# Performance work log

Hardware: AMD Instinct MI355X
Metric: run time of the kernel (lower is better)

## Reference

```python
import jax, jax.numpy as jnp
import numpy as np

E, M, K, I, TOPK = 8, 4096, 2048, 1408, 2
N = 2 * I  # gated: w1 produces [gate, up]


def setup_inputs() -> dict:
    key = jax.random.key(0)
    k1, k2, k3, k4, k5 = jax.random.split(key, 5)
    hidden_states = jax.random.normal(k1, (M, K), dtype=jnp.float32)
    w1 = jax.random.normal(k2, (E, N, K), dtype=jnp.float32) * 0.02
    w2 = jax.random.normal(k3, (E, K, I), dtype=jnp.float32) * 0.02
    raw = jax.random.uniform(k4, (M, TOPK), dtype=jnp.float32)
    topk_weights = raw / jnp.sum(raw, axis=-1, keepdims=True)  # router probs
    topk_ids = jax.random.randint(k5, (M, TOPK), 0, E, dtype=jnp.int32)
    return {
        "hidden_states": hidden_states,
        "w1": w1,
        "w2": w2,
        "topk_weights": topk_weights,
        "topk_ids": topk_ids,
    }


def reference(hidden_states, w1, w2, topk_weights, topk_ids):
    # MoE: permute -> grouped GEMM1 -> silu_and_mul -> grouped GEMM2 -> unpermute+reduce.
    # Dense-per-expert formulation (math-equivalent to grouped GEMM over routed tokens).
    # GEMM1: [E, M, N]
    h1 = jnp.einsum("mk,enk->emn", hidden_states, w1)
    gate, up = h1[..., :I], h1[..., I:]
    act = jax.nn.silu(gate) * up  # silu_and_mul, [E, M, I]
    # GEMM2: [E, M, K]
    y = jnp.einsum("emi,eki->emk", act, w2)
    # Unpermute: gather each token's topk expert outputs, apply router weights, reduce.
    y_tok = jnp.transpose(y, (1, 0, 2))  # [M, E, K]
    sel = jnp.take_along_axis(y_tok, topk_ids[:, :, None].astype(jnp.int32), axis=1)  # [M, topk, K]
    out = jnp.sum(sel * topk_weights[:, :, None], axis=1)  # [M, K]
    return out
```

## Files before the change

kernel.cpp:

```cpp
#include <hip/hip_runtime.h>
#include <hip/hip_bf16.h>
#include <stdint.h>

#define EXPERTS 8
#define MTOK 4096
#define KDIM 2048
#define IDIM 1408
#define NDIM 2816
#define CAP  8192

typedef __attribute__((ext_vector_type(8))) short bf16x8;
typedef __attribute__((ext_vector_type(4))) float f32x4;

__device__ __forceinline__ unsigned short f2bf(float x) {
    unsigned u = __float_as_uint(x);
    u = u + 0x7fffu + ((u >> 16) & 1u);
    return (unsigned short)(u >> 16);
}

__device__ __forceinline__ void gload16(const void* g, void* l) {
    __builtin_amdgcn_global_load_lds(
        (const __attribute__((address_space(1))) void*)g,
        (__attribute__((address_space(3))) void*)l, 16, 0, 0);
}

__global__ void __launch_bounds__(256) conv_bf16(const float* __restrict__ src,
                                                 unsigned short* __restrict__ dst, int n4) {
    int i = blockIdx.x * 256 + threadIdx.x;
    int st = gridDim.x * 256;
    for (; i < n4; i += st) {
        float4 v = reinterpret_cast<const float4*>(src)[i];
        ushort4 r;
        r.x = f2bf(v.x); r.y = f2bf(v.y); r.z = f2bf(v.z); r.w = f2bf(v.w);
        reinterpret_cast<ushort4*>(dst)[i] = r;
    }
}

__global__ void __launch_bounds__(256) router(const float* __restrict__ tw,
                                              const int* __restrict__ ids,
                                              int* __restrict__ tok, float* __restrict__ wgt,
                                              int* __restrict__ cnt) {
    int m = blockIdx.x * 256 + threadIdx.x;
    if (m >= MTOK) return;
#pragma unroll
    for (int t = 0; t < 2; t++) {
        int e = ids[m * 2 + t];
        int slot = atomicAdd(&cnt[e], 1);
        tok[e * CAP + slot] = m;
        wgt[e * CAP + slot] = tw[m * 2 + t];
    }
}

__global__ void scan_off(const int* __restrict__ cnt, int* __restrict__ off) {
    if (threadIdx.x == 0) {
        int s = 0;
        for (int e = 0; e < EXPERTS; e++) { off[e] = s; s += cnt[e]; }
    }
}


__global__ void __launch_bounds__(256) gemm1_silu(
    const unsigned short* __restrict__ hsb,
    const unsigned short* __restrict__ w1b,
    const int* __restrict__ tok,
    const int* __restrict__ cnt,
    const int* __restrict__ off,
    unsigned short* __restrict__ act) {
    const int bid = blockIdx.x;
    const int e = bid & 7;
    const int j = bid >> 3;
    const int rb = j / 22;
    const int cb = j - rb * 22;
    const int cnt_e = cnt[e];
    if (rb * 128 >= cnt_e) return;
    const int off_e = off[e];

    __shared__ unsigned short As[128 * 64];
    __shared__ unsigned short Bs[128 * 64];
    __shared__ int toks[128];

    const int tid = threadIdx.x;
    const int w = tid >> 6, lane = tid & 63;
    if (tid < 128) {
        int slot = rb * 128 + tid;
        toks[tid] = (slot < cnt_e) ? tok[e * CAP + slot] : 0;
    }
    __syncthreads();

    size_t sA[4], sB[4]; int dD[4];
    const size_t w1base = (size_t)e * NDIM * KDIM;
#pragma unroll
    for (int c = 0; c < 4; c++) {
        int i = c * 256 + tid;
        int row = i >> 3, g = (i & 7) ^ (row & 7);
        sA[c] = (size_t)toks[row] * KDIM + g * 8;
        int G = row >> 4;
        int wrow = ((G & 1) ? IDIM : 0) + cb * 64 + (G >> 1) * 16 + (row & 15);
        sB[c] = w1base + (size_t)wrow * KDIM + g * 8;
        dD[c] = i * 16;
    }

    const int wr = w >> 1, wc = w & 1;
    const int l16 = lane & 15, lg = lane >> 4;

    f32x4 acc[4][4];
#pragma unroll
    for (int m = 0; m < 4; m++)
#pragma unroll
        for (int n = 0; n < 4; n++) acc[m][n] = {0.f, 0.f, 0.f, 0.f};

    char* Ab = (char*)As;
    char* Bb = (char*)Bs;

    for (int kt = 0; kt < KDIM / 64; ++kt) {
        const int kof = kt * 64;
#pragma unroll
        for (int c = 0; c < 4; c++) gload16(hsb + sA[c] + kof, Ab + dD[c]);
#pragma unroll
        for (int c = 0; c < 4; c++) gload16(w1b + sB[c] + kof, Bb + dD[c]);
        __syncthreads();

#pragma unroll
        for (int h = 0; h < 2; h++) {
            bf16x8 a[4], b[4];
#pragma unroll
            for (int m = 0; m < 4; m++) {
                int r = wr * 64 + m * 16 + l16;
                a[m] = *reinterpret_cast<bf16x8*>(Ab + r * 128 + (((h * 4 + lg) ^ (r & 7)) * 16));
            }
#pragma unroll
            for (int n = 0; n < 4; n++) {
                int r = wc * 64 + n * 16 + l16;
                b[n] = *reinterpret_cast<bf16x8*>(Bb + r * 128 + (((h * 4 + lg) ^ (r & 7)) * 16));
            }
#pragma unroll
            for (int m = 0; m < 4; m++)
#pragma unroll
                for (int n = 0; n < 4; n++)
                    acc[m][n] = __builtin_amdgcn_mfma_f32_16x16x32_bf16(a[m], b[n], acc[m][n], 0, 0, 0);
        }
        __syncthreads();
    }

#pragma unroll
    for (int m = 0; m < 4; m++) {
#pragma unroll
        for (int np = 0; np < 2; np++) {
            f32x4 g4 = acc[m][np * 2];
            f32x4 u4 = acc[m][np * 2 + 1];
            int icol = cb * 64 + (wc * 2 + np) * 16 + l16;
#pragma unroll
            for (int j2 = 0; j2 < 4; j2++) {
                int grow = rb * 128 + wr * 64 + m * 16 + lg * 4 + j2;
                if (grow < cnt_e) {
                    float gt = g4[j2], up = u4[j2];
                    float s = gt / (1.f + __expf(-gt));
                    act[(size_t)(off_e + grow) * IDIM + icol] = f2bf(s * up);
                }
            }
        }
    }
}

__global__ void __launch_bounds__(256) gemm2_scatter(
    const unsigned short* __restrict__ act,
    const unsigned short* __restrict__ w2b,
    const int* __restrict__ tok,
    const float* __restrict__ wgt,
    const int* __restrict__ cnt,
    const int* __restrict__ off,
    float* __restrict__ out) {
    const int bid = blockIdx.x;
    const int e = bid & 7;
    const int j = bid >> 3;
    const int rb = j >> 4;
    const int cb = j & 15;
    const int cnt_e = cnt[e];
    if (rb * 128 >= cnt_e) return;
    const int off_e = off[e];

    __shared__ unsigned short As[128 * 64];
    __shared__ unsigned short Bs[128 * 64];
    __shared__ int toks[128];
    __shared__ float wgts[128];

    const int tid = threadIdx.x;
    const int w = tid >> 6, lane = tid & 63;
    if (tid < 128) {
        int slot = rb * 128 + tid;
        bool v = slot < cnt_e;
        toks[tid] = v ? tok[e * CAP + slot] : 0;
        wgts[tid] = v ? wgt[e * CAP + slot] : 0.f;
    }
    __syncthreads();

    size_t sA[4], sB[4]; int dD[4];
    const size_t w2base = (size_t)e * KDIM * IDIM;
#pragma unroll
    for (int c = 0; c < 4; c++) {
        int i = c * 256 + tid;
        int row = i >> 3, g = (i & 7) ^ (row & 7);
        int s = rb * 128 + row;
        sA[c] = (size_t)(off_e + (s < cnt_e ? s : 0)) * IDIM + g * 8;
        sB[c] = w2base + (size_t)(cb * 128 + row) * IDIM + g * 8;
        dD[c] = i * 16;
    }

    const int wr = w >> 1, wc = w & 1;
    const int l16 = lane & 15, lg = lane >> 4;

    f32x4 acc[4][4];
#pragma unroll
    for (int m = 0; m < 4; m++)
#pragma unroll
        for (int n = 0; n < 4; n++) acc[m][n] = {0.f, 0.f, 0.f, 0.f};

    char* Ab = (char*)As;
    char* Bb = (char*)Bs;

    for (int kt = 0; kt < IDIM / 64; ++kt) {
        const int kof = kt * 64;
#pragma unroll
        for (int c = 0; c < 4; c++) gload16(act + sA[c] + kof, Ab + dD[c]);
#pragma unroll
        for (int c = 0; c < 4; c++) gload16(w2b + sB[c] + kof, Bb + dD[c]);
        __syncthreads();

#pragma unroll
        for (int h = 0; h < 2; h++) {
            bf16x8 a[4], b[4];
#pragma unroll
            for (int m = 0; m < 4; m++) {
                int r = wr * 64 + m * 16 + l16;
                a[m] = *reinterpret_cast<bf16x8*>(Ab + r * 128 + (((h * 4 + lg) ^ (r & 7)) * 16));
            }
#pragma unroll
            for (int n = 0; n < 4; n++) {
                int r = wc * 64 + n * 16 + l16;
                b[n] = *reinterpret_cast<bf16x8*>(Bb + r * 128 + (((h * 4 + lg) ^ (r & 7)) * 16));
            }
#pragma unroll
            for (int m = 0; m < 4; m++)
#pragma unroll
                for (int n = 0; n < 4; n++)
                    acc[m][n] = __builtin_amdgcn_mfma_f32_16x16x32_bf16(a[m], b[n], acc[m][n], 0, 0, 0);
        }
        __syncthreads();
    }

#pragma unroll
    for (int m = 0; m < 4; m++) {
#pragma unroll
        for (int n = 0; n < 4; n++) {
            int kcol = cb * 128 + wc * 64 + n * 16 + l16;
#pragma unroll
            for (int j2 = 0; j2 < 4; j2++) {
                int lrow = wr * 64 + m * 16 + lg * 4 + j2;
                if (rb * 128 + lrow < cnt_e) {
                    atomicAdd(&out[(size_t)toks[lrow] * KDIM + kcol],
                              wgts[lrow] * acc[m][n][j2]);
                }
            }
        }
    }
}

extern "C" void kernel_launch(void* const* d_in, const int* in_sizes, int n_in,
                              void* d_out, int out_size, void* d_ws, size_t ws_size,
                              hipStream_t stream) {
    const float* hs  = (const float*)d_in[0];
    const float* w1  = (const float*)d_in[1];
    const float* w2  = (const float*)d_in[2];
    const float* tw  = (const float*)d_in[3];
    const int*   ids = (const int*)d_in[4];
    float* out = (float*)d_out;

    char* ws = (char*)d_ws;
    unsigned short* w1b  = (unsigned short*)(ws);
    unsigned short* w2b  = (unsigned short*)(ws + 92274688ull);
    unsigned short* hsb  = (unsigned short*)(ws + 138412032ull);
    unsigned short* actb = (unsigned short*)(ws + 155189248ull);
    int*   tokb = (int*)  (ws + 178257920ull);
    float* wgtb = (float*)(ws + 178520064ull);
    int*   cntb = (int*)  (ws + 178782208ull);
    int*   offb = (int*)  (ws + 178782240ull);

    hipMemsetAsync(d_out, 0, (size_t)MTOK * KDIM * sizeof(float), stream);
    hipMemsetAsync(cntb, 0, 64, stream);

    conv_bf16<<<4096, 256, 0, stream>>>(w1, w1b, EXPERTS * NDIM * KDIM / 4);
    conv_bf16<<<2048, 256, 0, stream>>>(w2, w2b, EXPERTS * KDIM * IDIM / 4);
    conv_bf16<<<1024, 256, 0, stream>>>(hs, hsb, MTOK * KDIM / 4);

    router<<<MTOK / 256, 256, 0, stream>>>(tw, ids, tokb, wgtb, cntb);
    scan_off<<<1, 64, 0, stream>>>(cntb, offb);

    gemm1_silu<<<dim3(22 * 64 * 8, 1, 1), 256, 0, stream>>>(hsb, w1b, tokb, cntb, offb, actb);
    gemm2_scatter<<<dim3(16 * 64 * 8, 1, 1), 256, 0, stream>>>(actb, w2b, tokb, wgtb, cntb, offb, out);
}
```

Baseline: 415.1 us.

## Reshape GEMM tiles to 256x64 with K-step 32 and per-wave row ownership

Both grouped GEMMs move from a 128x128 tile with a 64-wide K step to a 256-row by 64-column tile with a 32-wide K step. Each wave now owns 64 rows and the full 64 columns, and the shared-memory swizzle and load mapping are rebuilt for 64-byte rows. This cuts LDS per block, which may allow more blocks per CU, and loads each weight tile once for more tokens. In exchange it doubles the number of K iterations and barriers, and the 256-row tiles waste more work on each expert's partial last tile.

```diff
diff --git a/kernel.cpp b/kernel.cpp
--- a/kernel.cpp
+++ b/kernel.cpp
@@ -69,39 +69,55 @@
     const int bid = blockIdx.x;
     const int e = bid & 7;
     const int j = bid >> 3;
-    const int rb = j / 22;
-    const int cb = j - rb * 22;
+    const int rb = j / 44;
+    const int cb = j - rb * 44;
     const int cnt_e = cnt[e];
-    if (rb * 128 >= cnt_e) return;
+    if (rb * 256 >= cnt_e) return;
     const int off_e = off[e];
-
-    __shared__ unsigned short As[128 * 64];
-    __shared__ unsigned short Bs[128 * 64];
-    __shared__ int toks[128];
+    const int NT = KDIM / 32;
+
+    __shared__ __align__(16) char smem[20480];
+    __shared__ int toks[256];
 
     const int tid = threadIdx.x;
     const int w = tid >> 6, lane = tid & 63;
-    if (tid < 128) {
-        int slot = rb * 128 + tid;
+    {
+        int slot = rb * 256 + tid;
         toks[tid] = (slot < cnt_e) ? tok[e * CAP + slot] : 0;
     }
     __syncthreads();
 
-    size_t sA[4], sB[4]; int dD[4];
+    size_t sA[4]; int dA[4];
+#pragma unroll
+    for (int k = 0; k < 4; k++) {
+        int c = k * 256 + tid;
+        int row = c >> 2, g = (c & 3) ^ ((row >> 1) & 3);
+        sA[k] = (size_t)toks[row] * KDIM + g * 8;
+        dA[k] = c * 16;
+    }
     const size_t w1base = (size_t)e * NDIM * KDIM;
-#pragma unroll
-    for (int c = 0; c < 4; c++) {
-        int i = c * 256 + tid;
-        int row = i >> 3, g = (i & 7) ^ (row & 7);
-        sA[c] = (size_t)toks[row] * KDIM + g * 8;
+    size_t sB0; int dB0;
+    {
+        int c = tid;
+        int row = c >> 2, g = (c & 3) ^ ((row >> 1) & 3);
         int G = row >> 4;
-        int wrow = ((G & 1) ? IDIM : 0) + cb * 64 + (G >> 1) * 16 + (row & 15);
-        sB[c] = w1base + (size_t)wrow * KDIM + g * 8;
-        dD[c] = i * 16;
-    }
-
-    const int wr = w >> 1, wc = w & 1;
+        int wrow = ((G & 1) ? IDIM : 0) + cb * 32 + (G >> 1) * 16 + (row & 15);
+        sB0 = w1base + (size_t)wrow * KDIM + g * 8;
+        dB0 = 16384 + c * 16;
+    }
+
     const int l16 = lane & 15, lg = lane >> 4;
+    int aoff[4], boff[4];
+#pragma unroll
+    for (int m = 0; m < 4; m++) {
+        int r = w * 64 + m * 16 + l16;
+        aoff[m] = r * 64 + ((lg ^ ((r >> 1) & 3)) * 16);
+    }
+#pragma unroll
+    for (int n = 0; n < 4; n++) {
+        int r = n * 16 + l16;
+        boff[n] = 16384 + r * 64 + ((lg ^ ((r >> 1) & 3)) * 16);
+    }
 
     f32x4 acc[4][4];
 #pragma unroll
@@ -109,36 +125,23 @@
 #pragma unroll
         for (int n = 0; n < 4; n++) acc[m][n] = {0.f, 0.f, 0.f, 0.f};
 
-    char* Ab = (char*)As;
-    char* Bb = (char*)Bs;
-
-    for (int kt = 0; kt < KDIM / 64; ++kt) {
-        const int kof = kt * 64;
-#pragma unroll
-        for (int c = 0; c < 4; c++) gload16(hsb + sA[c] + kof, Ab + dD[c]);
-#pragma unroll
-        for (int c = 0; c < 4; c++) gload16(w1b + sB[c] + kof, Bb + dD[c]);
+    for (int kt = 0; kt < NT; ++kt) {
+        const int kof = kt * 32;
+#pragma unroll
+        for (int k = 0; k < 4; k++) gload16(hsb + sA[k] + kof, smem + dA[k]);
+        gload16(w1b + sB0 + kof, smem + dB0);
         __syncthreads();
 
-#pragma unroll
-        for (int h = 0; h < 2; h++) {
-            bf16x8 a[4], b[4];
-#pragma unroll
-            for (int m = 0; m < 4; m++) {
-                int r = wr * 64 + m * 16 + l16;
-                a[m] = *reinterpret_cast<bf16x8*>(Ab + r * 128 + (((h * 4 + lg) ^ (r & 7)) * 16));
-            }
-#pragma unroll
-            for (int n = 0; n < 4; n++) {
-                int r = wc * 64 + n * 16 + l16;
-                b[n] = *reinterpret_cast<bf16x8*>(Bb + r * 128 + (((h * 4 + lg) ^ (r & 7)) * 16));
-            }
-#pragma unroll
-            for (int m = 0; m < 4; m++)
-#pragma unroll
-                for (int n = 0; n < 4; n++)
-                    acc[m][n] = __builtin_amdgcn_mfma_f32_16x16x32_bf16(a[m], b[n], acc[m][n], 0, 0, 0);
-        }
+        bf16x8 af[4], bf[4];
+#pragma unroll
+        for (int m = 0; m < 4; m++) af[m] = *(const bf16x8*)(smem + aoff[m]);
+#pragma unroll
+        for (int n = 0; n < 4; n++) bf[n] = *(const bf16x8*)(smem + boff[n]);
+#pragma unroll
+        for (int m = 0; m < 4; m++)
+#pragma unroll
+            for (int n = 0; n < 4; n++)
+                acc[m][n] = __builtin_amdgcn_mfma_f32_16x16x32_bf16(af[m], bf[n], acc[m][n], 0, 0, 0);
         __syncthreads();
     }
 
@@ -148,10 +151,10 @@
         for (int np = 0; np < 2; np++) {
             f32x4 g4 = acc[m][np * 2];
             f32x4 u4 = acc[m][np * 2 + 1];
-            int icol = cb * 64 + (wc * 2 + np) * 16 + l16;
+            int icol = cb * 32 + np * 16 + l16;
 #pragma unroll
             for (int j2 = 0; j2 < 4; j2++) {
-                int grow = rb * 128 + wr * 64 + m * 16 + lg * 4 + j2;
+                int grow = rb * 256 + w * 64 + m * 16 + lg * 4 + j2;
                 if (grow < cnt_e) {
                     float gt = g4[j2], up = u4[j2];
                     float s = gt / (1.f + __expf(-gt));
@@ -173,41 +176,57 @@
     const int bid = blockIdx.x;
     const int e = bid & 7;
     const int j = bid >> 3;
-    const int rb = j >> 4;
-    const int cb = j & 15;
+    const int rb = j >> 5;
+    const int cb = j & 31;
     const int cnt_e = cnt[e];
-    if (rb * 128 >= cnt_e) return;
+    if (rb * 256 >= cnt_e) return;
     const int off_e = off[e];
-
-    __shared__ unsigned short As[128 * 64];
-    __shared__ unsigned short Bs[128 * 64];
-    __shared__ int toks[128];
-    __shared__ float wgts[128];
+    const int NT = IDIM / 32;
+
+    __shared__ __align__(16) char smem[20480];
+    __shared__ int toks[256];
+    __shared__ float wgts[256];
 
     const int tid = threadIdx.x;
     const int w = tid >> 6, lane = tid & 63;
-    if (tid < 128) {
-        int slot = rb * 128 + tid;
+    {
+        int slot = rb * 256 + tid;
         bool v = slot < cnt_e;
         toks[tid] = v ? tok[e * CAP + slot] : 0;
         wgts[tid] = v ? wgt[e * CAP + slot] : 0.f;
     }
     __syncthreads();
 
-    size_t sA[4], sB[4]; int dD[4];
+    size_t sA[4]; int dA[4];
+#pragma unroll
+    for (int k = 0; k < 4; k++) {
+        int c = k * 256 + tid;
+        int row = c >> 2, g = (c & 3) ^ ((row >> 1) & 3);
+        int s = rb * 256 + row;
+        sA[k] = (size_t)(off_e + (s < cnt_e ? s : 0)) * IDIM + g * 8;
+        dA[k] = c * 16;
+    }
     const size_t w2base = (size_t)e * KDIM * IDIM;
-#pragma unroll
-    for (int c = 0; c < 4; c++) {
-        int i = c * 256 + tid;
-        int row = i >> 3, g = (i & 7) ^ (row & 7);
-        int s = rb * 128 + row;
-        sA[c] = (size_t)(off_e + (s < cnt_e ? s : 0)) * IDIM + g * 8;
-        sB[c] = w2base + (size_t)(cb * 128 + row) * IDIM + g * 8;
-        dD[c] = i * 16;
-    }
-
-    const int wr = w >> 1, wc = w & 1;
+    size_t sB0; int dB0;
+    {
+        int c = tid;
+        int row = c >> 2, g = (c & 3) ^ ((row >> 1) & 3);
+        sB0 = w2base + (size_t)(cb * 64 + row) * IDIM + g * 8;
+        dB0 = 16384 + c * 16;
+    }
+
     const int l16 = lane & 15, lg = lane >> 4;
+    int aoff[4], boff[4];
+#pragma unroll
+    for (int m = 0; m < 4; m++) {
+        int r = w * 64 + m * 16 + l16;
+        aoff[m] = r * 64 + ((lg ^ ((r >> 1) & 3)) * 16);
+    }
+#pragma unroll
+    for (int n = 0; n < 4; n++) {
+        int r = n * 16 + l16;
+        boff[n] = 16384 + r * 64 + ((lg ^ ((r >> 1) & 3)) * 16);
+    }
 
     f32x4 acc[4][4];
 #pragma unroll
@@ -215,36 +234,23 @@
 #pragma unroll
         for (int n = 0; n < 4; n++) acc[m][n] = {0.f, 0.f, 0.f, 0.f};
 
-    char* Ab = (char*)As;
-    char* Bb = (char*)Bs;
-
-    for (int kt = 0; kt < IDIM / 64; ++kt) {
-        const int kof = kt * 64;
-#pragma unroll
-        for (int c = 0; c < 4; c++) gload16(act + sA[c] + kof, Ab + dD[c]);
-#pragma unroll
-        for (int c = 0; c < 4; c++) gload16(w2b + sB[c] + kof, Bb + dD[c]);
+    for (int kt = 0; kt < NT; ++kt) {
+        const int kof = kt * 32;
+#pragma unroll
+        for (int k = 0; k < 4; k++) gload16(act + sA[k] + kof, smem + dA[k]);
+        gload16(w2b + sB0 + kof, smem + dB0);
         __syncthreads();
 
-#pragma unroll
-        for (int h = 0; h < 2; h++) {
-            bf16x8 a[4], b[4];
-#pragma unroll
-            for (int m = 0; m < 4; m++) {
-                int r = wr * 64 + m * 16 + l16;
-                a[m] = *reinterpret_cast<bf16x8*>(Ab + r * 128 + (((h * 4 + lg) ^ (r & 7)) * 16));
-            }
-#pragma unroll
-            for (int n = 0; n < 4; n++) {
-                int r = wc * 64 + n * 16 + l16;
-                b[n] = *reinterpret_cast<bf16x8*>(Bb + r * 128 + (((h * 4 + lg) ^ (r & 7)) * 16));
-            }
-#pragma unroll
-            for (int m = 0; m < 4; m++)
-#pragma unroll
-                for (int n = 0; n < 4; n++)
-                    acc[m][n] = __builtin_amdgcn_mfma_f32_16x16x32_bf16(a[m], b[n], acc[m][n], 0, 0, 0);
-        }
+        bf16x8 af[4], bf[4];
+#pragma unroll
+        for (int m = 0; m < 4; m++) af[m] = *(const bf16x8*)(smem + aoff[m]);
+#pragma unroll
+        for (int n = 0; n < 4; n++) bf[n] = *(const bf16x8*)(smem + boff[n]);
+#pragma unroll
+        for (int m = 0; m < 4; m++)
+#pragma unroll
+            for (int n = 0; n < 4; n++)
+                acc[m][n] = __builtin_amdgcn_mfma_f32_16x16x32_bf16(af[m], bf[n], acc[m][n], 0, 0, 0);
         __syncthreads();
     }
 
@@ -252,11 +258,11 @@
     for (int m = 0; m < 4; m++) {
 #pragma unroll
         for (int n = 0; n < 4; n++) {
-            int kcol = cb * 128 + wc * 64 + n * 16 + l16;
+            int kcol = cb * 64 + n * 16 + l16;
 #pragma unroll
             for (int j2 = 0; j2 < 4; j2++) {
-                int lrow = wr * 64 + m * 16 + lg * 4 + j2;
-                if (rb * 128 + lrow < cnt_e) {
+                int lrow = w * 64 + m * 16 + lg * 4 + j2;
+                if (rb * 256 + lrow < cnt_e) {
                     atomicAdd(&out[(size_t)toks[lrow] * KDIM + kcol],
                               wgts[lrow] * acc[m][n][j2]);
                 }
@@ -295,6 +301,6 @@
     router<<<MTOK / 256, 256, 0, stream>>>(tw, ids, tokb, wgtb, cntb);
     scan_off<<<1, 64, 0, stream>>>(cntb, offb);
 
-    gemm1_silu<<<dim3(22 * 64 * 8, 1, 1), 256, 0, stream>>>(hsb, w1b, tokb, cntb, offb, actb);
-    gemm2_scatter<<<dim3(16 * 64 * 8, 1, 1), 256, 0, stream>>>(actb, w2b, tokb, wgtb, cntb, offb, out);
-}
+    gemm1_silu<<<dim3(44 * 32 * 8, 1, 1), 256, 0, stream>>>(hsb, w1b, tokb, cntb, offb, actb);
+    gemm2_scatter<<<dim3(32 * 32 * 8, 1, 1), 256, 0, stream>>>(actb, w2b, tokb, wgtb, cntb, offb, out);
+}
```

Result: slower. 431.0 us (+3.8%).
